# Optimization experiments

Hardware: AMD Instinct MI355X
Metric: run time of the kernel (lower is better)

Reference implementation:

```python
import jax, jax.numpy as jnp
import numpy as np

S = 0.7071067811865476  # 1/sqrt(2), Haar filter coefficient
J = 2                   # wavelet_level
NUM_HEADS = 8
GROUPS = 32             # min(32, 256 // 4)
EPS = 1e-5


def _dwt2(x):
    # single-level 2D Haar DWT; symmetric mode with even sizes needs no padding
    lo = (x[..., ::2] + x[..., 1::2]) * S          # along W
    hi = (x[..., ::2] - x[..., 1::2]) * S
    ll = (lo[..., ::2, :] + lo[..., 1::2, :]) * S  # along H
    lh = (lo[..., ::2, :] - lo[..., 1::2, :]) * S
    hl = (hi[..., ::2, :] + hi[..., 1::2, :]) * S
    hh = (hi[..., ::2, :] - hi[..., 1::2, :]) * S
    return ll, jnp.stack([lh, hl, hh], axis=2)     # yh: [B,C,3,h,w]


def _ileave(a, b, axis):
    # interleave a,b along `axis` (inverse of stride-2 split)
    sh = list(a.shape)
    sh[axis] *= 2
    return jnp.stack([a, b], axis=axis + 1).reshape(sh)


def _idwt2(ll, bands):
    lh, hl, hh = bands[:, :, 0], bands[:, :, 1], bands[:, :, 2]
    lo = _ileave((ll + lh) * S, (ll - lh) * S, 2)  # undo H transform
    hi = _ileave((hl + hh) * S, (hl - hh) * S, 2)
    return _ileave((lo + hi) * S, (lo - hi) * S, 3)  # undo W transform


def _dwt(x):
    yh = []
    ll = x
    for _ in range(J):
        ll, b = _dwt2(ll)
        yh.append(b)
    return ll, yh


def _idwt(ll, yh):
    for b in reversed(yh):
        ll = _idwt2(ll, b)
    return ll


def _conv1x1(x, W, b):
    return jnp.einsum('nchw,oc->nohw', x, W) + b[None, :, None, None]


def _groupnorm(x, gamma, beta):
    B, C, H, W = x.shape
    g = x.reshape(B, GROUPS, C // GROUPS, H, W)
    mu = g.mean(axis=(2, 3, 4), keepdims=True)
    var = g.var(axis=(2, 3, 4), keepdims=True)
    g = (g - mu) * jax.lax.rsqrt(var + EPS)
    return g.reshape(B, C, H, W) * gamma[None, :, None, None] + beta[None, :, None, None]


def setup_inputs() -> dict:
    key = jax.random.key(0)
    ks = jax.random.split(key, 8)
    B, N, C, H, W = 2, 4, 256, 128, 128
    f32 = jnp.float32
    return {
        'query': jax.random.normal(ks[0], (B, C, H, W), f32),
        'key_value_multi': jax.random.normal(ks[1], (B, N, C, H, W), f32),
        'value_multi': jax.random.normal(ks[2], (B, N, C, H, W), f32),
        'Wq': jax.random.normal(ks[3], (C, C), f32) * 0.02,
        'bq': jnp.zeros((C,), f32),
        'Wk': jax.random.normal(ks[4], (C, C), f32) * 0.02,
        'bk': jnp.zeros((C,), f32),
        'Wv': jax.random.normal(ks[5], (C, C), f32) * 0.02,
        'bv': jnp.zeros((C,), f32),
        'Wp': jax.random.normal(ks[6], (C, C), f32) * 0.02,
        'bp': jnp.zeros((C,), f32),
        'gamma': jnp.ones((C,), f32),
        'beta': jnp.zeros((C,), f32),
    }


def reference(query, key_value_multi, value_multi, Wq, bq, Wk, bk, Wv, bv, Wp, bp, gamma, beta):
    B, N, C, H, W = key_value_multi.shape
    q_yl, q_yh = _dwt(query)
    hl_, wl_ = q_yl.shape[-2:]
    # torch cats per-anchor batches along dim 0 -> flat order is (n, b)
    kv = jnp.transpose(key_value_multi, (1, 0, 2, 3, 4)).reshape(N * B, C, H, W)
    kv_yl, _ = _dwt(kv)  # kv high bands are discarded by the original
    q = _conv1x1(jnp.tile(q_yl, (N, 1, 1, 1)), Wq, bq)
    k = _conv1x1(kv_yl, Wk, bk)
    v = _conv1x1(kv_yl, Wv, bv)
    BN, hd, T = N * B, C // NUM_HEADS, hl_ * wl_

    def heads(t):
        return t.reshape(BN, NUM_HEADS, hd, T).transpose(0, 1, 3, 2)  # [BN,h,T,d]

    qh, kh, vh = heads(q), heads(k), heads(v)
    attn = jax.nn.softmax(jnp.einsum('bhsd,bhtd->bhst', qh, kh) * (hd ** -0.5), axis=-1)
    out = jnp.einsum('bhst,bhtd->bhsd', attn, vh)
    out = out.transpose(0, 1, 3, 2).reshape(BN, C, hl_, wl_)
    out = _conv1x1(out, Wp, bp)
    # faithful to torch: flat (n,b)-ordered tensor viewed as (B,N,...) then mean over dim 1
    out = out.reshape(B, N, C, hl_, wl_).mean(axis=1)
    out_full = _idwt(out, q_yh)[:, :, :H, :W]
    return _groupnorm(out_full, gamma, beta) + query
```

## Files before the change

### kernel.cpp

```cpp
#include <hip/hip_runtime.h>


typedef float f32x16 __attribute__((ext_vector_type(16)));
typedef short s16x8 __attribute__((ext_vector_type(8)));

static __device__ __forceinline__ unsigned f2bf_bits(float x) {
  unsigned u = __float_as_uint(x);
  return (u + 0x7fffu + ((u >> 16) & 1u)) >> 16;
}
static __device__ __forceinline__ unsigned pack2(float a, float b) {
  return f2bf_bits(a) | (f2bf_bits(b) << 16);
}
static __device__ __forceinline__ float bflo(unsigned u) {
  return __uint_as_float(u << 16);
}
static __device__ __forceinline__ float bfhi(unsigned u) {
  return __uint_as_float(u & 0xffff0000u);
}
static __device__ __forceinline__ int swz(int byte) {
  return byte ^ (((byte >> 7) & 7) << 4);
}

__global__ __launch_bounds__(256) void dwt_kernel(const float* __restrict__ query,
    const float* __restrict__ kvm, unsigned short* __restrict__ qll,
    unsigned short* __restrict__ kvll, float* __restrict__ partial) {
  int bid = blockIdx.x;
  if (bid < 2048) {
    int idx = bid * 256 + threadIdx.x;
    int bc = idx >> 10;
    int t  = idx & 1023;
    int i = t >> 5, j = t & 31;
    const float* xp = query + (size_t)bc * 16384;
    float s = 0.f, e = 0.f;
#pragma unroll
    for (int rr = 0; rr < 4; ++rr) {
      float4 v = *reinterpret_cast<const float4*>(xp + (4 * i + rr) * 128 + 4 * j);
      s += (v.x + v.y) + (v.z + v.w);
      e += (v.x * v.x + v.y * v.y) + (v.z * v.z + v.w * v.w);
    }
    qll[idx] = (unsigned short)f2bf_bits(0.25f * s);
    __shared__ float red[256];
    red[threadIdx.x] = e;
    __syncthreads();
    for (int off = 128; off > 0; off >>= 1) {
      if (threadIdx.x < off) red[threadIdx.x] += red[threadIdx.x + off];
      __syncthreads();
    }
    if (threadIdx.x == 0) partial[bid] = red[0];
  } else {
    int idx = (bid - 2048) * 256 + threadIdx.x;
    int bc = idx >> 10;
    int t  = idx & 1023;
    int i = t >> 5, j2 = t & 31;
    int jj = bc >> 8, c = bc & 255;
    int n = jj >> 1, b = jj & 1;
    const float* xp = kvm + ((size_t)(b * 4 + n) * 256 + c) * 16384;
    float s = 0.f;
#pragma unroll
    for (int rr = 0; rr < 4; ++rr) {
      float4 v = *reinterpret_cast<const float4*>(xp + (4 * i + rr) * 128 + 4 * j2);
      s += (v.x + v.y) + (v.z + v.w);
    }
    kvll[idx] = (unsigned short)f2bf_bits(0.25f * s);
  }
}

static __device__ __forceinline__ void stage_w(const float* __restrict__ Wm,
    char* ldsA, int o0, int k0, int oA, int kqA, float sc) {
  const float* wp = Wm + (size_t)(o0 + oA) * 256 + k0 + kqA;
  float4 w0 = *reinterpret_cast<const float4*>(wp);
  float4 w1 = *reinterpret_cast<const float4*>(wp + 4);
  float4 w2 = *reinterpret_cast<const float4*>(wp + 8);
  float4 w3 = *reinterpret_cast<const float4*>(wp + 12);
  union { s16x8 v; unsigned u[4]; } a0, a1;
  a0.u[0] = pack2(sc * w0.x, sc * w0.y); a0.u[1] = pack2(sc * w0.z, sc * w0.w);
  a0.u[2] = pack2(sc * w1.x, sc * w1.y); a0.u[3] = pack2(sc * w1.z, sc * w1.w);
  a1.u[0] = pack2(sc * w2.x, sc * w2.y); a1.u[1] = pack2(sc * w2.z, sc * w2.w);
  a1.u[2] = pack2(sc * w3.x, sc * w3.y); a1.u[3] = pack2(sc * w3.z, sc * w3.w);
  int byte0 = oA * 128 + kqA * 2;
  *reinterpret_cast<s16x8*>(ldsA + swz(byte0))      = a0.v;
  *reinterpret_cast<s16x8*>(ldsA + swz(byte0 + 16)) = a1.v;
}

static __device__ __forceinline__ void stage_x_bf(const unsigned short* __restrict__ Xp,
    char* ldsB, int k0, int t0, int tB, int kg0) {
#pragma unroll
  for (int rep = 0; rep < 2; ++rep) {
    int kg = kg0 + rep * 4;
    const unsigned short* xp = Xp + (size_t)(k0 + kg * 8) * 1024 + t0 + tB;
    union { s16x8 v; unsigned u[4]; } b;
#pragma unroll
    for (int e2 = 0; e2 < 4; ++e2) {
      unsigned lo = xp[(size_t)(2 * e2) * 1024];
      unsigned hi2 = xp[(size_t)(2 * e2 + 1) * 1024];
      b.u[e2] = lo | (hi2 << 16);
    }
    *reinterpret_cast<s16x8*>(ldsB + swz(tB * 128 + kg * 16)) = b.v;
  }
}

static __device__ __forceinline__ void stage_x_m4p(const unsigned* __restrict__ Ap,
    char* ldsB, int k0, int t0, int tB, int kg0) {
#pragma unroll
  for (int rep = 0; rep < 2; ++rep) {
    int kg = kg0 + rep * 4;
    const unsigned* xp = Ap + (size_t)(k0 / 2 + kg * 4) * 1024 + t0 + tB;
    union { s16x8 v; unsigned u[4]; } b;
#pragma unroll
    for (int e2 = 0; e2 < 4; ++e2) {
      unsigned a0 = xp[(size_t)e2 * 1024];
      unsigned a1 = xp[(size_t)e2 * 1024 + 131072];
      unsigned a2 = xp[(size_t)e2 * 1024 + 262144];
      unsigned a3 = xp[(size_t)e2 * 1024 + 393216];
      float lo = 0.25f * ((bflo(a0) + bflo(a1)) + (bflo(a2) + bflo(a3)));
      float hi2 = 0.25f * ((bfhi(a0) + bfhi(a1)) + (bfhi(a2) + bfhi(a3)));
      b.u[e2] = pack2(lo, hi2);
    }
    *reinterpret_cast<s16x8*>(ldsB + swz(tB * 128 + kg * 16)) = b.v;
  }
}

__global__ __launch_bounds__(256) void conv_qkv_kernel(
    const unsigned short* __restrict__ qll, const unsigned short* __restrict__ kvll,
    const float* __restrict__ Wq, const float* __restrict__ bq,
    const float* __restrict__ Wk, const float* __restrict__ bk,
    const float* __restrict__ Wv, const float* __restrict__ bv,
    unsigned* __restrict__ qbp, unsigned* __restrict__ kbp,
    unsigned short* __restrict__ vb) {
  const int tid = threadIdx.x;
  const int hi = (tid >> 5) & 1;
  const int ln = tid & 31;
  const int w = tid >> 6;
  const int o_off = (w >> 1) * 32;
  const int t_off = (w & 1) * 32;
  const int t0 = blockIdx.x * 64;
  const int o0 = blockIdx.y * 64;
  const int z = blockIdx.z;

  __shared__ __align__(16) char lds[24576];
  char* ldsA  = lds;
  char* ldsA2 = lds + 8192;
  char* ldsB  = lds + 16384;

  const int oA = tid >> 2;
  const int kqA = (tid & 3) * 16;
  const int tB = tid & 63;
  const int kg0 = tid >> 6;

  if (z < 2) {
    const float S = 0.17677669529663687f;
    const unsigned short* Xp = qll + (size_t)z * 262144;
    f32x16 acc;
#pragma unroll
    for (int r = 0; r < 16; ++r) acc[r] = 0.f;
    for (int kk = 0; kk < 4; ++kk) {
      const int k0 = kk * 64;
      stage_w(Wq, ldsA, o0, k0, oA, kqA, S);
      stage_x_bf(Xp, ldsB, k0, t0, tB, kg0);
      __syncthreads();
#pragma unroll
      for (int ks = 0; ks < 64; ks += 16) {
        s16x8 af = *reinterpret_cast<const s16x8*>(ldsA + swz((o_off + ln) * 128 + ks * 2 + hi * 16));
        s16x8 bf = *reinterpret_cast<const s16x8*>(ldsB + swz((t_off + ln) * 128 + ks * 2 + hi * 16));
        acc = __builtin_amdgcn_mfma_f32_32x32x16_bf16(af, bf, acc, 0, 0, 0);
      }
      __syncthreads();
    }
    unsigned* Yp = qbp + (size_t)z * 131072;
#pragma unroll
    for (int r = 0; r < 16; r += 2) {
      int o = o_off + (r & 3) + 8 * (r >> 2) + 4 * hi;
      float b0 = S * bq[o0 + o], b1 = S * bq[o0 + o + 1];
      Yp[(size_t)((o0 + o) >> 1) * 1024 + t0 + t_off + ln] =
          pack2(acc[r] + b0, acc[r + 1] + b1);
    }
  } else {
    const int jj = z - 2;
    const unsigned short* Xp = kvll + (size_t)jj * 262144;
    f32x16 acck, accv;
#pragma unroll
    for (int r = 0; r < 16; ++r) { acck[r] = 0.f; accv[r] = 0.f; }
    for (int kk = 0; kk < 4; ++kk) {
      const int k0 = kk * 64;
      stage_w(Wk, ldsA,  o0, k0, oA, kqA, 1.f);
      stage_w(Wv, ldsA2, o0, k0, oA, kqA, 1.f);
      stage_x_bf(Xp, ldsB, k0, t0, tB, kg0);
      __syncthreads();
#pragma unroll
      for (int ks = 0; ks < 64; ks += 16) {
        s16x8 bf  = *reinterpret_cast<const s16x8*>(ldsB  + swz((t_off + ln) * 128 + ks * 2 + hi * 16));
        s16x8 afk = *reinterpret_cast<const s16x8*>(ldsA  + swz((o_off + ln) * 128 + ks * 2 + hi * 16));
        s16x8 afv = *reinterpret_cast<const s16x8*>(ldsA2 + swz((o_off + ln) * 128 + ks * 2 + hi * 16));
        acck = __builtin_amdgcn_mfma_f32_32x32x16_bf16(afk, bf, acck, 0, 0, 0);
        accv = __builtin_amdgcn_mfma_f32_32x32x16_bf16(afv, bf, accv, 0, 0, 0);
      }
      __syncthreads();
    }
    unsigned* Yk = kbp + (size_t)jj * 131072;
    unsigned short* Yv = vb + (size_t)jj * 262144;
#pragma unroll
    for (int r = 0; r < 16; r += 2) {
      int o = o_off + (r & 3) + 8 * (r >> 2) + 4 * hi;
      Yk[(size_t)((o0 + o) >> 1) * 1024 + t0 + t_off + ln] =
          pack2(acck[r] + bk[o0 + o], acck[r + 1] + bk[o0 + o + 1]);
    }
#pragma unroll
    for (int r = 0; r < 16; ++r) {
      int o = o_off + (r & 3) + 8 * (r >> 2) + 4 * hi;
      Yv[(size_t)(o0 + o) * 1024 + t0 + t_off + ln] =
          (unsigned short)f2bf_bits(accv[r] + bv[o0 + o]);
    }
  }
}

__global__ __launch_bounds__(256) void attn_mfma_kernel(
    const unsigned* __restrict__ qbp, const unsigned* __restrict__ kbp,
    const unsigned short* __restrict__ vb, unsigned* __restrict__ aop) {
  const int tid = threadIdx.x;
  const int w   = tid >> 6;
  const int hi  = (tid >> 5) & 1;
  const int ln  = tid & 31;
  const int jh  = blockIdx.x >> 3;
  const int qg  = blockIdx.x & 7;
  const int qbase = (qg * 4 + w) * 32;
  const int j = jh >> 3, h = jh & 7;
  const unsigned* qp = qbp + (size_t)((j & 1) * 8 + h) * 16384;
  const unsigned* kp = kbp + (size_t)jh * 16384;
  const unsigned short* vp = vb + (size_t)jh * 32768;

  __shared__ unsigned KpL[2][544];
  __shared__ unsigned VpL[2][544];
  __shared__ float tileT[4][1056];

  const int sdp = tid >> 5;
  const int st  = tid & 31;
  const int svd = tid >> 4;
  const int svt = tid & 15;

  s16x8 Qf[2];
#pragma unroll
  for (int c = 0; c < 2; ++c) {
    union { s16x8 v; unsigned u[4]; } u;
#pragma unroll
    for (int e2 = 0; e2 < 4; ++e2)
      u.u[e2] = qp[(size_t)(c * 8 + hi * 4 + e2) * 1024 + qbase + ln];
    Qf[c] = u.v;
  }

  f32x16 acc;
#pragma unroll
  for (int r = 0; r < 16; ++r) acc[r] = 0.f;
  float m = -1e30f, lsum = 0.f;

  {
    KpL[0][st * 17 + sdp]     = kp[(size_t)sdp * 1024 + st];
    KpL[0][st * 17 + sdp + 8] = kp[(size_t)(sdp + 8) * 1024 + st];
    VpL[0][svd * 17 + svt] =
        *reinterpret_cast<const unsigned*>(vp + (size_t)svd * 1024 + 2 * svt);
    VpL[0][(svd + 16) * 17 + svt] =
        *reinterpret_cast<const unsigned*>(vp + (size_t)(svd + 16) * 1024 + 2 * svt);
  }
  __syncthreads();

  for (int tile = 0; tile < 32; ++tile) {
    const int cur = tile & 1;
    unsigned nk0 = 0, nk1 = 0, nv0 = 0, nv1 = 0;
    if (tile < 31) {
      const int kn = (tile + 1) * 32;
      nk0 = kp[(size_t)sdp * 1024 + kn + st];
      nk1 = kp[(size_t)(sdp + 8) * 1024 + kn + st];
      nv0 = *reinterpret_cast<const unsigned*>(vp + (size_t)svd * 1024 + kn + 2 * svt);
      nv1 = *reinterpret_cast<const unsigned*>(vp + (size_t)(svd + 16) * 1024 + kn + 2 * svt);
    }

    s16x8 Kf[2];
#pragma unroll
    for (int c = 0; c < 2; ++c) {
      union { s16x8 v; unsigned u[4]; } u;
#pragma unroll
      for (int e = 0; e < 4; ++e)
        u.u[e] = KpL[cur][ln * 17 + c * 8 + hi * 4 + e];
      Kf[c] = u.v;
    }
    f32x16 S;
#pragma unroll
    for (int r = 0; r < 16; ++r) S[r] = 0.f;
    S = __builtin_amdgcn_mfma_f32_32x32x16_bf16(Kf[0], Qf[0], S, 0, 0, 0);
    S = __builtin_amdgcn_mfma_f32_32x32x16_bf16(Kf[1], Qf[1], S, 0, 0, 0);

    float tmax = S[0];
#pragma unroll
    for (int r = 1; r < 16; ++r) tmax = fmaxf(tmax, S[r]);
    tmax = fmaxf(tmax, __shfl_xor(tmax, 32));
    if (__any(tmax > m + 6.f)) {
      float nm = fmaxf(m, tmax);
      float f  = __expf(m - nm);
      m = nm;
      lsum *= f;
      int fi = __float_as_int(f);
#pragma unroll
      for (int r = 0; r < 16; ++r) {
        int row = (r & 3) + 8 * (r >> 2) + 4 * hi;
        float fr = __int_as_float(__builtin_amdgcn_ds_bpermute(row * 4, fi));
        acc[r] *= fr;
      }
    }
    float p[16];
#pragma unroll
    for (int r = 0; r < 16; ++r) {
      p[r] = __expf(S[r] - m);
      lsum += p[r];
    }
    unsigned P[8];
#pragma unroll
    for (int i = 0; i < 8; ++i) P[i] = pack2(p[2 * i], p[2 * i + 1]);

#pragma unroll
    for (int c = 0; c < 2; ++c) {
      unsigned p0 = P[4 * c + 0], p1 = P[4 * c + 1];
      unsigned p2 = P[4 * c + 2], p3 = P[4 * c + 3];
      unsigned s0 = (unsigned)__shfl_xor((int)p0, 32);
      unsigned s1 = (unsigned)__shfl_xor((int)p1, 32);
      unsigned s2 = (unsigned)__shfl_xor((int)p2, 32);
      unsigned s3 = (unsigned)__shfl_xor((int)p3, 32);
      union { s16x8 v; unsigned u[4]; } pa;
      pa.u[0] = hi ? s2 : p0;
      pa.u[1] = hi ? s3 : p1;
      pa.u[2] = hi ? p2 : s0;
      pa.u[3] = hi ? p3 : s1;
      union { s16x8 v; unsigned u[4]; } vf;
#pragma unroll
      for (int e = 0; e < 4; ++e)
        vf.u[e] = VpL[cur][ln * 17 + c * 8 + hi * 4 + e];
      acc = __builtin_amdgcn_mfma_f32_32x32x16_bf16(pa.v, vf.v, acc, 0, 0, 0);
    }

    if (tile < 31) {
      const int nxt = cur ^ 1;
      KpL[nxt][st * 17 + sdp]     = nk0;
      KpL[nxt][st * 17 + sdp + 8] = nk1;
      VpL[nxt][svd * 17 + svt]        = nv0;
      VpL[nxt][(svd + 16) * 17 + svt] = nv1;
    }
    __syncthreads();
  }

  float ltot = lsum + __shfl_xor(lsum, 32);
  float inv  = 1.f / ltot;

  float* tw = tileT[w];
#pragma unroll
  for (int r = 0; r < 16; ++r) {
    int row = (r & 3) + 8 * (r >> 2) + 4 * hi;
    tw[row * 33 + ln] = acc[r];
  }
  __syncthreads();
  unsigned* aw = aop + (size_t)jh * 16384;
#pragma unroll
  for (int pass = 0; pass < 8; ++pass) {
    int dp = pass * 2 + hi;
    float v0 = tw[ln * 33 + 2 * dp] * inv;
    float v1 = tw[ln * 33 + 2 * dp + 1] * inv;
    aw[(size_t)dp * 1024 + qbase + ln] = pack2(v0, v1);
  }
}

__global__ __launch_bounds__(256) void conv_pm_kernel(const unsigned* __restrict__ aop,
    const float* __restrict__ Wm, const float* __restrict__ bias,
    float* __restrict__ Y) {
  const int tid = threadIdx.x;
  const int hi = (tid >> 5) & 1;
  const int ln = tid & 31;
  const int w = tid >> 6;
  const int o_off = (w >> 1) * 32;
  const int t_off = (w & 1) * 32;
  const int t0 = blockIdx.x * 64;
  const int o0 = blockIdx.y * 64;
  const int bp = blockIdx.z;
  const unsigned* Ap = aop + (size_t)bp * 524288;

  __shared__ __align__(16) char lds[16384];
  char* ldsA = lds;
  char* ldsB = lds + 8192;

  f32x16 acc;
#pragma unroll
  for (int r = 0; r < 16; ++r) acc[r] = 0.f;

  const int oA = tid >> 2;
  const int kqA = (tid & 3) * 16;
  const int tB = tid & 63;
  const int kg0 = tid >> 6;

  for (int kk = 0; kk < 4; ++kk) {
    const int k0 = kk * 64;
    stage_w(Wm, ldsA, o0, k0, oA, kqA, 1.f);
    stage_x_m4p(Ap, ldsB, k0, t0, tB, kg0);
    __syncthreads();
#pragma unroll
    for (int ks = 0; ks < 64; ks += 16) {
      s16x8 af = *reinterpret_cast<const s16x8*>(ldsA + swz((o_off + ln) * 128 + ks * 2 + hi * 16));
      s16x8 bf = *reinterpret_cast<const s16x8*>(ldsB + swz((t_off + ln) * 128 + ks * 2 + hi * 16));
      acc = __builtin_amdgcn_mfma_f32_32x32x16_bf16(af, bf, acc, 0, 0, 0);
    }
    __syncthreads();
  }

  size_t ybase = ((size_t)bp * 256 + o0) * 1024 + t0;
#pragma unroll
  for (int r = 0; r < 16; ++r) {
    int o = o_off + (r & 3) + 8 * (r >> 2) + 4 * hi;
    Y[ybase + (size_t)o * 1024 + t_off + ln] = acc[r] + bias[o0 + o];
  }
}

__global__ __launch_bounds__(256) void stats64_kernel(const float* __restrict__ mb,
    const unsigned short* __restrict__ qll, const float* __restrict__ partial,
    float* __restrict__ stats) {
  int g = blockIdx.x, tid = threadIdx.x;
  size_t base = (size_t)(g >> 5) * 262144 + (size_t)(g & 31) * 8192;
  const float4* p = reinterpret_cast<const float4*>(mb + base);
  float s = 0.f, s2 = 0.f;
  for (int e = tid; e < 2048; e += 256) {
    float4 v = p[e];
    s  += (v.x + v.y) + (v.z + v.w);
    s2 += (v.x * v.x + v.y * v.y) + (v.z * v.z + v.w * v.w);
  }
  const uint2* qp2 = reinterpret_cast<const uint2*>(qll + base);
  for (int e = tid; e < 2048; e += 256) {
    uint2 q = qp2[e];
    float a = bflo(q.x), b2 = bfhi(q.x), c2 = bflo(q.y), d2 = bfhi(q.y);
    s2 -= (a * a + b2 * b2) + (c2 * c2 + d2 * d2);
  }
  if (tid < 32) {
    int cc = tid >> 2, q = tid & 3;
    s2 += partial[(((g >> 5) * 256 + (g & 31) * 8 + cc) << 2) + q];
  }
  __shared__ float ls[256], ls2[256];
  ls[tid] = s; ls2[tid] = s2;
  __syncthreads();
  for (int off = 128; off > 0; off >>= 1) {
    if (tid < off) { ls[tid] += ls[tid + off]; ls2[tid] += ls2[tid + off]; }
    __syncthreads();
  }
  if (tid == 0) {
    float mean = 4.f * ls[0] * (1.f / 131072.f);
    float ex2  = ls2[0] * (1.f / 131072.f);
    float var  = ex2 - mean * mean;
    stats[g * 2]     = mean;
    stats[g * 2 + 1] = rsqrtf(var + 1e-5f);
  }
}

__global__ __launch_bounds__(256) void idwt_gn_kernel(const float* __restrict__ mb,
    const unsigned short* __restrict__ qll, const float* __restrict__ query,
    const float* __restrict__ stats, const float* __restrict__ gamma,
    const float* __restrict__ beta, float* __restrict__ out) {
  int idx = blockIdx.x * 256 + threadIdx.x;
  int bc = idx >> 10;
  int t  = idx & 1023;
  int i = t >> 5, j = t & 31;
  int c = bc & 255;
  int g = (bc >> 8) * 32 + (c >> 3);
  float mean = stats[2 * g], rstd = stats[2 * g + 1];
  float a_s = rstd * gamma[c];
  float be  = beta[c];
  float delta = 0.25f * (mb[idx] - bflo((unsigned)qll[idx]));
  float k1 = 1.f + a_s;
  float k2 = (delta - mean) * a_s + be;
  const float* qp = query + (size_t)bc * 16384;
  float* op = out + (size_t)bc * 16384;
#pragma unroll
  for (int rr = 0; rr < 4; ++rr) {
    int off = (4 * i + rr) * 128 + 4 * j;
    float4 q = *reinterpret_cast<const float4*>(qp + off);
    float4 o;
    o.x = q.x * k1 + k2;
    o.y = q.y * k1 + k2;
    o.z = q.z * k1 + k2;
    o.w = q.w * k1 + k2;
    *reinterpret_cast<float4*>(op + off) = o;
  }
}

extern "C" void kernel_launch(void* const* d_in, const int* in_sizes, int n_in,
                              void* d_out, int out_size, void* d_ws, size_t ws_size,
                              hipStream_t stream) {
  const float* query = (const float*)d_in[0];
  const float* kvm   = (const float*)d_in[1];
  const float* Wq = (const float*)d_in[3];
  const float* bq = (const float*)d_in[4];
  const float* Wk = (const float*)d_in[5];
  const float* bk = (const float*)d_in[6];
  const float* Wv = (const float*)d_in[7];
  const float* bv = (const float*)d_in[8];
  const float* Wp = (const float*)d_in[9];
  const float* bp = (const float*)d_in[10];
  const float* gamma = (const float*)d_in[11];
  const float* beta  = (const float*)d_in[12];
  float* out = (float*)d_out;
  float* ws  = (float*)d_ws;

  if (ws_size < (size_t)5244032 * 4) return;

  unsigned short* qll  = (unsigned short*)ws;
  unsigned short* kvll = (unsigned short*)(ws + 262144);
  unsigned*       qbp  = (unsigned*)(ws + 1310720);
  unsigned*       kbp  = (unsigned*)(ws + 1572864);
  unsigned short* vb   = (unsigned short*)(ws + 2621440);
  unsigned*       aop  = (unsigned*)(ws + 3670016);
  float*          mb   = ws + 4718592;
  float*       partial = ws + 5242880;
  float*         stats = ws + 5244928 - 2048 + 2048;
  stats = partial + 2048;

  dwt_kernel<<<10240, 256, 0, stream>>>(query, kvm, qll, kvll, partial);

  conv_qkv_kernel<<<dim3(16, 4, 10), 256, 0, stream>>>(
      qll, kvll, Wq, bq, Wk, bk, Wv, bv, qbp, kbp, vb);

  attn_mfma_kernel<<<512, 256, 0, stream>>>(qbp, kbp, vb, aop);

  conv_pm_kernel<<<dim3(16, 4, 2), 256, 0, stream>>>(aop, Wp, bp, mb);
  stats64_kernel<<<64, 256, 0, stream>>>(mb, qll, partial, stats);

  idwt_gn_kernel<<<2048, 256, 0, stream>>>(mb, qll, query, stats,
                                           gamma, beta, out);
}
```

Before: 96.60 us.

## Fuse GroupNorm statistics into projection conv and final kernel, drop stats kernel

The separate stats64 kernel is removed. The output-projection conv now reduces per-group sums and squared sums of its results into per-block partials. The idwt/groupnorm kernel finishes the reduction per block from those partials plus the DWT energy partials. The DWT kernel subtracts the squared LL term itself and uses wave-shuffle reductions instead of a shared-memory tree. This saves one launch and a reread of mb and qll, at the cost of redundant small reductions in every final block and a reordered floating-point summation.

```diff
diff --git a/kernel.cpp b/kernel.cpp
--- a/kernel.cpp
+++ b/kernel.cpp
@@ -38,15 +38,17 @@
       s += (v.x + v.y) + (v.z + v.w);
       e += (v.x * v.x + v.y * v.y) + (v.z * v.z + v.w * v.w);
     }
-    qll[idx] = (unsigned short)f2bf_bits(0.25f * s);
-    __shared__ float red[256];
-    red[threadIdx.x] = e;
+    unsigned bits = f2bf_bits(0.25f * s);
+    qll[idx] = (unsigned short)bits;
+    float qv = __uint_as_float(bits << 16);
+    e -= qv * qv;
+#pragma unroll
+    for (int o = 32; o > 0; o >>= 1) e += __shfl_xor(e, o);
+    __shared__ float red[4];
+    if ((threadIdx.x & 63) == 0) red[threadIdx.x >> 6] = e;
     __syncthreads();
-    for (int off = 128; off > 0; off >>= 1) {
-      if (threadIdx.x < off) red[threadIdx.x] += red[threadIdx.x + off];
-      __syncthreads();
-    }
-    if (threadIdx.x == 0) partial[bid] = red[0];
+    if (threadIdx.x == 0)
+      partial[bid] = (red[0] + red[1]) + (red[2] + red[3]);
   } else {
     int idx = (bid - 2048) * 256 + threadIdx.x;
     int bc = idx >> 10;
@@ -367,7 +369,7 @@
 
 __global__ __launch_bounds__(256) void conv_pm_kernel(const unsigned* __restrict__ aop,
     const float* __restrict__ Wm, const float* __restrict__ bias,
-    float* __restrict__ Y) {
+    float* __restrict__ Y, float* __restrict__ pm_part) {
   const int tid = threadIdx.x;
   const int hi = (tid >> 5) & 1;
   const int ln = tid & 31;
@@ -407,62 +409,81 @@
   }
 
   size_t ybase = ((size_t)bp * 256 + o0) * 1024 + t0;
+  float gs[4] = {0.f, 0.f, 0.f, 0.f}, gs2[4] = {0.f, 0.f, 0.f, 0.f};
 #pragma unroll
   for (int r = 0; r < 16; ++r) {
     int o = o_off + (r & 3) + 8 * (r >> 2) + 4 * hi;
-    Y[ybase + (size_t)o * 1024 + t_off + ln] = acc[r] + bias[o0 + o];
-  }
-}
-
-__global__ __launch_bounds__(256) void stats64_kernel(const float* __restrict__ mb,
-    const unsigned short* __restrict__ qll, const float* __restrict__ partial,
-    float* __restrict__ stats) {
-  int g = blockIdx.x, tid = threadIdx.x;
-  size_t base = (size_t)(g >> 5) * 262144 + (size_t)(g & 31) * 8192;
-  const float4* p = reinterpret_cast<const float4*>(mb + base);
-  float s = 0.f, s2 = 0.f;
-  for (int e = tid; e < 2048; e += 256) {
-    float4 v = p[e];
-    s  += (v.x + v.y) + (v.z + v.w);
-    s2 += (v.x * v.x + v.y * v.y) + (v.z * v.z + v.w * v.w);
-  }
-  const uint2* qp2 = reinterpret_cast<const uint2*>(qll + base);
-  for (int e = tid; e < 2048; e += 256) {
-    uint2 q = qp2[e];
-    float a = bflo(q.x), b2 = bfhi(q.x), c2 = bflo(q.y), d2 = bfhi(q.y);
-    s2 -= (a * a + b2 * b2) + (c2 * c2 + d2 * d2);
-  }
-  if (tid < 32) {
-    int cc = tid >> 2, q = tid & 3;
-    s2 += partial[(((g >> 5) * 256 + (g & 31) * 8 + cc) << 2) + q];
-  }
-  __shared__ float ls[256], ls2[256];
-  ls[tid] = s; ls2[tid] = s2;
+    float y = acc[r] + bias[o0 + o];
+    Y[ybase + (size_t)o * 1024 + t_off + ln] = y;
+    gs[r >> 2] += y;
+    gs2[r >> 2] += y * y;
+  }
+#pragma unroll
+  for (int off = 32; off > 0; off >>= 1) {
+#pragma unroll
+    for (int g2 = 0; g2 < 4; ++g2) {
+      gs[g2]  += __shfl_xor(gs[g2], off);
+      gs2[g2] += __shfl_xor(gs2[g2], off);
+    }
+  }
+  float* lf = reinterpret_cast<float*>(lds);
+  if ((tid & 63) == 0) {
+#pragma unroll
+    for (int g2 = 0; g2 < 4; ++g2) {
+      lf[w * 8 + g2 * 2]     = gs[g2];
+      lf[w * 8 + g2 * 2 + 1] = gs2[g2];
+    }
+  }
   __syncthreads();
-  for (int off = 128; off > 0; off >>= 1) {
-    if (tid < off) { ls[tid] += ls[tid + off]; ls2[tid] += ls2[tid + off]; }
-    __syncthreads();
-  }
-  if (tid == 0) {
-    float mean = 4.f * ls[0] * (1.f / 131072.f);
-    float ex2  = ls2[0] * (1.f / 131072.f);
-    float var  = ex2 - mean * mean;
-    stats[g * 2]     = mean;
-    stats[g * 2 + 1] = rsqrtf(var + 1e-5f);
+  if (tid < 16) {
+    int gl = tid >> 1, sidx = tid & 1;
+    int wa = (gl < 4) ? 0 : 2;
+    float v = lf[wa * 8 + (gl & 3) * 2 + sidx] +
+              lf[(wa + 1) * 8 + (gl & 3) * 2 + sidx];
+    int gg = bp * 32 + blockIdx.y * 8 + gl;
+    pm_part[(gg * 16 + blockIdx.x) * 2 + sidx] = v;
   }
 }
 
 __global__ __launch_bounds__(256) void idwt_gn_kernel(const float* __restrict__ mb,
     const unsigned short* __restrict__ qll, const float* __restrict__ query,
-    const float* __restrict__ stats, const float* __restrict__ gamma,
-    const float* __restrict__ beta, float* __restrict__ out) {
+    const float* __restrict__ pm_part, const float* __restrict__ partial,
+    const float* __restrict__ gamma, const float* __restrict__ beta,
+    float* __restrict__ out) {
+  int bc = blockIdx.x >> 2;
+  int c = bc & 255;
+  int g = (bc >> 8) * 32 + (c >> 3);
+
+  __shared__ float sstat[2];
+  if (threadIdx.x < 64) {
+    int l = threadIdx.x;
+    float s = 0.f, s2 = 0.f;
+    if (l < 16) {
+      float2 pp = *reinterpret_cast<const float2*>(pm_part + (g * 16 + l) * 2);
+      s = pp.x; s2 = pp.y;
+    } else if (l < 48) {
+      int q = l - 16;
+      int blk = (((g >> 5) * 256 + (g & 31) * 8 + (q >> 2)) << 2) + (q & 3);
+      s2 = partial[blk];
+    }
+#pragma unroll
+    for (int off = 32; off > 0; off >>= 1) {
+      s  += __shfl_xor(s, off);
+      s2 += __shfl_xor(s2, off);
+    }
+    if (l == 0) {
+      float mean = 4.f * s * (1.f / 131072.f);
+      float ex2  = s2 * (1.f / 131072.f);
+      sstat[0] = mean;
+      sstat[1] = rsqrtf(ex2 - mean * mean + 1e-5f);
+    }
+  }
+  __syncthreads();
+  float mean = sstat[0], rstd = sstat[1];
+
   int idx = blockIdx.x * 256 + threadIdx.x;
-  int bc = idx >> 10;
   int t  = idx & 1023;
   int i = t >> 5, j = t & 31;
-  int c = bc & 255;
-  int g = (bc >> 8) * 32 + (c >> 3);
-  float mean = stats[2 * g], rstd = stats[2 * g + 1];
   float a_s = rstd * gamma[c];
   float be  = beta[c];
   float delta = 0.25f * (mb[idx] - bflo((unsigned)qll[idx]));
@@ -501,7 +522,7 @@
   float* out = (float*)d_out;
   float* ws  = (float*)d_ws;
 
-  if (ws_size < (size_t)5244032 * 4) return;
+  if (ws_size < (size_t)5246976 * 4) return;
 
   unsigned short* qll  = (unsigned short*)ws;
   unsigned short* kvll = (unsigned short*)(ws + 262144);
@@ -511,8 +532,7 @@
   unsigned*       aop  = (unsigned*)(ws + 3670016);
   float*          mb   = ws + 4718592;
   float*       partial = ws + 5242880;
-  float*         stats = ws + 5244928 - 2048 + 2048;
-  stats = partial + 2048;
+  float*       pm_part = partial + 2048;
 
   dwt_kernel<<<10240, 256, 0, stream>>>(query, kvm, qll, kvll, partial);
 
@@ -521,9 +541,8 @@
 
   attn_mfma_kernel<<<512, 256, 0, stream>>>(qbp, kbp, vb, aop);
 
-  conv_pm_kernel<<<dim3(16, 4, 2), 256, 0, stream>>>(aop, Wp, bp, mb);
-  stats64_kernel<<<64, 256, 0, stream>>>(mb, qll, partial, stats);
-
-  idwt_gn_kernel<<<2048, 256, 0, stream>>>(mb, qll, query, stats,
+  conv_pm_kernel<<<dim3(16, 4, 2), 256, 0, stream>>>(aop, Wp, bp, mb, pm_part);
+
+  idwt_gn_kernel<<<2048, 256, 0, stream>>>(mb, qll, query, pm_part, partial,
                                            gamma, beta, out);
 }
```

Result: faster. 91.73 us (-5.0%).
